# Optimization experiments

Hardware: AMD Instinct MI355X
Metric: run time of the kernel (lower is better)

The kernel has to match this reference:

```python
import jax, jax.numpy as jnp
import numpy as np
import math

B, H, W, DM = 4, 64, 64, 96
DS, DCONV, EXPAND = 16, 3, 2
DI = EXPAND * DM
DTR = math.ceil(DM / 16)
K = 4
HID = 4 * DI


def layernorm(x, g, b, eps=1e-5):
    m = x.mean(-1, keepdims=True)
    v = ((x - m) ** 2).mean(-1, keepdims=True)
    return (x - m) / jnp.sqrt(v + eps) * g + b


def dwconv(x, w, b=None):
    # x: (B,C,H,W), w: (C,1,kh,kw) depthwise, odd kernel => SAME padding == k//2
    out = jax.lax.conv_general_dilated(x, w, (1, 1), 'SAME',
                                       feature_group_count=x.shape[1],
                                       dimension_numbers=('NCHW', 'OIHW', 'NCHW'))
    if b is not None:
        out = out + b[None, :, None, None]
    return out


def ss2d_core(xc, x_proj_w, dt_projs_w, dt_projs_b, A_logs, Ds):
    # xc: (b, d_inner, h, w) -> (b, d_inner, L) summed over 4 scan directions
    b, c, h, w = xc.shape
    L = h * w
    x_hw = xc.reshape(b, c, L)
    x_wh = xc.transpose(0, 1, 3, 2).reshape(b, c, L)
    xs = jnp.stack([x_hw, x_wh], axis=1)                 # (b,2,c,L)
    xs = jnp.concatenate([xs, jnp.flip(xs, -1)], axis=1)  # (b,4,c,L)
    x_dbl = jnp.einsum('bkdl,kcd->bkcl', xs, x_proj_w)
    dts, Bs, Cs = jnp.split(x_dbl, [DTR, DTR + DS], axis=2)
    dts = jnp.einsum('bkrl,kdr->bkdl', dts, dt_projs_w)
    delta = jax.nn.softplus(dts + dt_projs_b[None, :, :, None])  # (b,K,c,L)
    A = -jnp.exp(A_logs).reshape(K, c, DS)                       # (K,c,n)

    def step(hst, inp):
        x_t, d_t, B_t, C_t = inp  # (b,K,c),(b,K,c),(b,K,n),(b,K,n)
        dA = jnp.exp(d_t[..., None] * A)                       # (b,K,c,n)
        hst = hst * dA + (d_t * x_t)[..., None] * B_t[:, :, None, :]
        y = jnp.einsum('bkdn,bkn->bkd', hst, C_t)
        return hst, y

    seq = (jnp.moveaxis(xs, -1, 0), jnp.moveaxis(delta, -1, 0),
           jnp.moveaxis(Bs, -1, 0), jnp.moveaxis(Cs, -1, 0))
    h0 = jnp.zeros((b, K, c, DS), xc.dtype)
    _, ys = jax.lax.scan(step, h0, seq)          # (L,b,K,c)
    ys = jnp.moveaxis(ys, 0, -1)                 # (b,K,c,L)
    ys = ys + Ds.reshape(K, c)[None, :, :, None] * xs
    y1 = ys[:, 0]
    inv = jnp.flip(ys[:, 2:4], -1)
    y2 = inv[:, 0]
    wh = ys[:, 1].reshape(b, c, w, h).swapaxes(2, 3).reshape(b, c, L)
    invwh = inv[:, 1].reshape(b, c, w, h).swapaxes(2, 3).reshape(b, c, L)
    return y1 + y2 + wh + invwh


def msffn(y, in_w, in_b, dw1, dw3, dw5, ln_g, ln_b, out_w, out_b):
    hcl = jax.nn.silu(y @ in_w.T + in_b)          # (b,h,w,HID)
    hc = hcl.transpose(0, 3, 1, 2)
    hc = hc + dwconv(hc, dw1) + dwconv(hc, dw3) + dwconv(hc, dw5)
    hn = layernorm(hc.transpose(0, 2, 3, 1), ln_g, ln_b)
    return hn @ out_w.T + out_b


def setup_inputs() -> dict:
    key = jax.random.key(0)
    ks = jax.random.split(key, 16)
    dt_init_std = DTR ** -0.5
    dt = jnp.exp(jax.random.uniform(ks[0], (K, DI)) * (math.log(0.1) - math.log(0.001)) + math.log(0.001))
    dt = jnp.clip(dt, 1e-4, None)
    inv_dt = dt + jnp.log(-jnp.expm1(-dt))          # softplus-inverse init for dt bias
    A_logs = jnp.tile(jnp.log(jnp.arange(1, DS + 1, dtype=jnp.float32))[None, :], (K * DI, 1))
    r = lambda i, sh, s: jax.random.normal(ks[i], sh, jnp.float32) * s
    return {
        'x': r(1, (B, H, W, DM), 1.0),
        'in_proj_w': r(2, (2 * DI, DM), DM ** -0.5),
        'conv_w': r(3, (DI, 1, DCONV, DCONV), 0.2),
        'conv_b': jnp.zeros((DI,), jnp.float32),
        'x_proj_w': r(4, (K, DTR + 2 * DS, DI), DI ** -0.5),
        'dt_projs_w': jax.random.uniform(ks[5], (K, DI, DTR), minval=-dt_init_std, maxval=dt_init_std),
        'dt_projs_b': inv_dt,
        'A_logs': A_logs,
        'Ds': jnp.ones((K * DI,), jnp.float32),
        'out_norm_g': jnp.ones((DI,), jnp.float32),
        'out_norm_b': jnp.zeros((DI,), jnp.float32),
        'out_proj_w': r(6, (DM, DI), DI ** -0.5),
        'ffn_in_w': r(7, (HID, DI), DI ** -0.5),
        'ffn_in_b': jnp.zeros((HID,), jnp.float32),
        'ffn_dw1': r(8, (HID, 1, 1, 1), 0.3),
        'ffn_dw3': r(9, (HID, 1, 3, 3), 0.2),
        'ffn_dw5': r(10, (HID, 1, 5, 5), 0.1),
        'ffn_ln_g': jnp.ones((HID,), jnp.float32),
        'ffn_ln_b': jnp.zeros((HID,), jnp.float32),
        'ffn_out_w': r(11, (DM, HID), HID ** -0.5),
        'ffn_out_b': jnp.zeros((DM,), jnp.float32),
        'skip_scale': jnp.ones((1,), jnp.float32),
    }


def reference(x, in_proj_w, conv_w, conv_b, x_proj_w, dt_projs_w, dt_projs_b, A_logs, Ds,
              out_norm_g, out_norm_b, out_proj_w, ffn_in_w, ffn_in_b, ffn_dw1, ffn_dw3,
              ffn_dw5, ffn_ln_g, ffn_ln_b, ffn_out_w, ffn_out_b, skip_scale):
    b, h, w, _ = x.shape
    xz = x @ in_proj_w.T                          # (b,h,w,2*DI)
    xi, z = jnp.split(xz, 2, axis=-1)
    xc = jax.nn.silu(dwconv(xi.transpose(0, 3, 1, 2), conv_w, conv_b))  # (b,DI,h,w)
    y = ss2d_core(xc, x_proj_w, dt_projs_w, dt_projs_b, A_logs, Ds)     # (b,DI,L)
    y = y.swapaxes(1, 2).reshape(b, h, w, DI)
    y = layernorm(y, out_norm_g, out_norm_b)
    y = y * jax.nn.silu(z)
    out = y @ out_proj_w.T
    ffn = msffn(y, ffn_in_w, ffn_in_b, ffn_dw1, ffn_dw3, ffn_dw5,
                ffn_ln_g, ffn_ln_b, ffn_out_w, ffn_out_b)
    return out + skip_scale * ffn
```

## Files before the change

### kernel.cpp

```cpp
#include <hip/hip_runtime.h>
#include <hip/hip_bf16.h>

constexpr int BB = 4, HH = 64, WW = 64, DMv = 96;
constexpr int DSn = 16, DIv = 192, DTRv = 6, KKv = 4, HIDv = 768;
constexpr int LL = 4096;
constexpr int NC = 64, CHK = LL / NC;
constexpr int NR = BB * LL;
constexpr int XDS = 40;

constexpr size_t S_xi   = (size_t)BB * LL * DIv;
constexpr size_t S_xdbl = (size_t)BB * KKv * LL * XDS;
constexpr size_t S_big  = (size_t)BB * KKv * LL * DIv;
constexpr size_t S_sp   = (size_t)BB * KKv * NC * DIv * DSn;

typedef __attribute__((ext_vector_type(8))) short short8;
typedef __attribute__((ext_vector_type(4))) short short4v;
typedef __attribute__((ext_vector_type(4))) float floatx4;

__device__ __forceinline__ float sigf(float x) { return 1.f / (1.f + __expf(-x)); }
__device__ __forceinline__ float softp(float x) {
  return (x > 20.f) ? x : __logf(1.f + __expf(x));
}
__device__ __forceinline__ short bfbits(float v) {
  __hip_bfloat16 h = __float2bfloat16(v);
  return *(short*)&h;
}

__device__ __forceinline__ int lmap(int k, int l) {
  int lr = (k & 2) ? (LL - 1 - l) : l;
  return (k & 1) ? (((lr & 63) << 6) | (lr >> 6)) : lr;
}

__global__ void k_wprep(const float* __restrict__ fiw, const float* __restrict__ opw,
                        const float* __restrict__ fow, const float* __restrict__ in_w,
                        const float* __restrict__ xpw, const float* __restrict__ x,
                        float* __restrict__ wt, float* __restrict__ xt,
                        short* __restrict__ fiwP, short* __restrict__ opwP,
                        short* __restrict__ fowP, short* __restrict__ wcatP) {
  int bx = blockIdx.x, t = threadIdx.x;
  __shared__ float smbuf[32 * 65];
  if (bx < 36) {
    int r0 = (bx / 3) * 32, c0 = (bx % 3) * 32;
    float (*tile)[33] = (float(*)[33])smbuf;
    int tc = t & 31, tr = t >> 5;
#pragma unroll
    for (int i = 0; i < 4; ++i)
      tile[tr + i * 8][tc] = in_w[(size_t)(r0 + tr + i * 8) * 96 + c0 + tc];
    __syncthreads();
#pragma unroll
    for (int i = 0; i < 4; ++i)
      wt[(size_t)(c0 + tr + i * 8) * 384 + r0 + tc] = tile[tc][tr + i * 8];
    return;
  }
  if (bx < 804) {
    int i4 = bx - 36;
    int r0 = (i4 / 3) * 64, k0 = (i4 % 3) * 32;
    float (*tile)[65] = (float(*)[65])smbuf;
#pragma unroll
    for (int ii = 0; ii < 8; ++ii) {
      int i = (t >> 5) + ii * 8, j = t & 31;
      tile[j][i] = x[(size_t)(r0 + i) * 96 + k0 + j];
    }
    __syncthreads();
#pragma unroll
    for (int jj = 0; jj < 8; ++jj) {
      int j = (t >> 6) + jj * 4, i = t & 63;
      xt[(size_t)(k0 + j) * NR + r0 + i] = tile[j][i];
    }
    return;
  }
  int lane = t & 63, ln16 = lane & 15, qd = lane >> 4;
  if (bx < 876) {
    int f = (bx - 804) * 4 + (t >> 6);
    int kt = f / 48, ntg = f % 48;
    int n = ntg * 16 + ln16;
#pragma unroll
    for (int j = 0; j < 8; ++j) {
      int k = kt * 32 + qd * 8 + j;
      fiwP[(size_t)f * 512 + lane * 8 + j] = bfbits(fiw[(size_t)n * DIv + k]);
    }
    return;
  }
  if (bx < 894) {
    int u = (bx - 876) * 4 + (t >> 6);
    int f = u >> 1, part = u & 1;
    int kt = f / 6, ntg = f % 6;
    int n = ntg * 16 + ln16;
#pragma unroll
    for (int j = 0; j < 8; ++j) {
      int k = kt * 32 + qd * 8 + j;
      float w = opw[(size_t)n * DIv + k];
      __hip_bfloat16 h = __float2bfloat16(w);
      float v = part ? (w - (float)h) : w;
      opwP[((size_t)(part * 36 + f)) * 512 + lane * 8 + j] = bfbits(v);
    }
    return;
  }
  if (bx < 966) {
    int u = (bx - 894) * 4 + (t >> 6);
    int f = u >> 1, part = u & 1;
    int kt = f / 6, ntg = f % 6;
    int n = ntg * 16 + ln16;
#pragma unroll
    for (int j = 0; j < 8; ++j) {
      int k = kt * 32 + qd * 8 + j;
      float w = fow[(size_t)n * HIDv + k];
      __hip_bfloat16 h = __float2bfloat16(w);
      float v = part ? (w - (float)h) : w;
      fowP[((size_t)(part * 144 + f)) * 512 + lane * 8 + j] = bfbits(v);
    }
    return;
  }
  {
    int u = (bx - 966) * 4 + (t >> 6);
    int p = u / 60, r = u % 60;
    int part = r / 30, r2 = r % 30;
    int kt = r2 / 5, g = r2 % 5;
    int n = g * 16 + ln16;
#pragma unroll
    for (int j = 0; j < 8; ++j) {
      int kd = kt * 32 + qd * 8 + j;
      float w = 0.f;
      if (n < 76) {
        int ksel = ((n >= 38) ? 2 : 0) + p;
        int cc = (n >= 38) ? n - 38 : n;
        w = xpw[(size_t)(ksel * 38 + cc) * DIv + kd];
      }
      __hip_bfloat16 h = __float2bfloat16(w);
      float v = part ? (w - (float)h) : w;
      wcatP[((size_t)(((p * 2 + part) * 6 + kt) * 5 + g)) * 512 + lane * 8 + j] = bfbits(v);
    }
  }
}

__global__ void k_inproj(const float* __restrict__ xt, const float* __restrict__ wt,
                         float* __restrict__ xi, float* __restrict__ z) {
  int t = threadIdx.x;
  int wv = t >> 6, lane = t & 63;
  int rq = blockIdx.x * 256 + wv * 64 + lane;
  int c0 = blockIdx.y * 8;
  const float4* xt4 = (const float4*)xt;
  float4 acc[8];
#pragma unroll
  for (int c = 0; c < 8; ++c) acc[c] = make_float4(0.f, 0.f, 0.f, 0.f);
  for (int k = 0; k < 96; ++k) {
    float4 xv = xt4[(size_t)k * (NR / 4) + rq];
    const float* wr = wt + k * 384 + c0;
#pragma unroll
    for (int c = 0; c < 8; ++c) {
      float w = wr[c];
      acc[c].x += w * xv.x; acc[c].y += w * xv.y;
      acc[c].z += w * xv.z; acc[c].w += w * xv.w;
    }
  }
  float* dst; int cc;
  if (c0 < DIv) { dst = xi; cc = c0; } else { dst = z; cc = c0 - DIv; }
#pragma unroll
  for (int li = 0; li < 4; ++li) {
    size_t row = (size_t)rq * 4 + li;
    float4 v0, v1;
    v0.x = (&acc[0].x)[li]; v0.y = (&acc[1].x)[li];
    v0.z = (&acc[2].x)[li]; v0.w = (&acc[3].x)[li];
    v1.x = (&acc[4].x)[li]; v1.y = (&acc[5].x)[li];
    v1.z = (&acc[6].x)[li]; v1.w = (&acc[7].x)[li];
    float4* o4 = (float4*)(dst + row * DIv + cc);
    o4[0] = v0; o4[1] = v1;
  }
}

constexpr int TW2 = 18;
__global__ void k_dwconv3(const float* __restrict__ xi, const float* __restrict__ cw,
                          const float* __restrict__ cb, float* __restrict__ xc,
                          short* __restrict__ xcBh, short* __restrict__ xcBl) {
  int tile = blockIdx.x;
  int cg = blockIdx.y, b = blockIdx.z;
  int t = threadIdx.x;
  int ti0 = (tile >> 2) * 16, tj0 = (tile & 3) * 16;
  __shared__ float sm[TW2 * TW2 * 32];

  for (int e = t; e < TW2 * TW2 * 32; e += 256) {
    int ec = e & 31;
    int sp = e >> 5;
    int hi = sp / TW2, hj = sp % TW2;
    int gi = ti0 + hi - 1, gj = tj0 + hj - 1;
    float v = 0.f;
    if ((unsigned)gi < (unsigned)HH && (unsigned)gj < (unsigned)WW)
      v = xi[((size_t)b * LL + gi * WW + gj) * DIv + cg * 32 + ec];
    sm[e] = v;
  }

  int c = t & 31, s0 = t >> 5;
  int cglob = cg * 32 + c;
  float wc[9];
#pragma unroll
  for (int j = 0; j < 9; ++j) wc[j] = cw[cglob * 9 + j];
  float bv = cb[cglob];
  __syncthreads();

  float res[32];
  for (int i = 0; i < 32; ++i) {
    int p = s0 + (i << 3);
    int r = p >> 4, q = p & 15;
    float s = bv;
#pragma unroll
    for (int di = 0; di < 3; ++di)
#pragma unroll
      for (int dj = 0; dj < 3; ++dj)
        s += sm[((r + di) * TW2 + (q + dj)) * 32 + c] * wc[di * 3 + dj];
    res[i] = s * sigf(s);
  }
  __syncthreads();
  for (int i = 0; i < 32; ++i) {
    int p = s0 + (i << 3);
    sm[p * 35 + c] = res[i];
  }
  __syncthreads();
  for (int it = 0; it < 32; ++it) {
    int e = it * 256 + t;
    int p = e >> 5, ec = e & 31;
    int l = (ti0 + (p >> 4)) * WW + tj0 + (p & 15);
    float v = sm[p * 35 + ec];
    size_t idx = ((size_t)b * LL + l) * DIv + cg * 32 + ec;
    xc[idx] = v;
    __hip_bfloat16 hh = __float2bfloat16(v);
    xcBh[idx] = *(short*)&hh;
    xcBl[idx] = bfbits(v - (float)hh);
  }
}

__global__ void k_xdblmf(const short* __restrict__ xcBh, const short* __restrict__ xcBl,
                         const short* __restrict__ wcatP, float* __restrict__ xdbl) {
  int t = threadIdx.x;
  int wv = t >> 6, lane = t & 63;
  int ln16 = lane & 15, qd = lane >> 4;
  int pb = blockIdx.y;
  int p = pb >> 2, b = pb & 3;
  int m0 = blockIdx.x * 64 + wv * 16;
  int r = m0 + ln16;
  int l = p ? (((r & 63) << 6) | (r >> 6)) : r;
  const short* ah = xcBh + ((size_t)(b * LL + l)) * DIv + qd * 8;
  const short* al = xcBl + ((size_t)(b * LL + l)) * DIv + qd * 8;
  floatx4 acc[5];
  floatx4 zero4 = {0.f, 0.f, 0.f, 0.f};
#pragma unroll
  for (int g = 0; g < 5; ++g) acc[g] = zero4;
#pragma unroll
  for (int kt = 0; kt < 6; ++kt) {
    short8 Ah = *(const short8*)(ah + kt * 32);
    short8 Al = *(const short8*)(al + kt * 32);
    const short* bh = wcatP + ((size_t)(((p * 2 + 0) * 6 + kt) * 5)) * 512 + lane * 8;
    const short* bl = wcatP + ((size_t)(((p * 2 + 1) * 6 + kt) * 5)) * 512 + lane * 8;
#pragma unroll
    for (int g = 0; g < 5; ++g) {
      short8 Bh = *(const short8*)(bh + (size_t)g * 512);
      short8 Bl = *(const short8*)(bl + (size_t)g * 512);
      acc[g] = __builtin_amdgcn_mfma_f32_16x16x32_bf16(Ah, Bh, acc[g], 0, 0, 0);
      acc[g] = __builtin_amdgcn_mfma_f32_16x16x32_bf16(Al, Bh, acc[g], 0, 0, 0);
      acc[g] = __builtin_amdgcn_mfma_f32_16x16x32_bf16(Ah, Bl, acc[g], 0, 0, 0);
    }
  }
#pragma unroll
  for (int g = 0; g < 5; ++g) {
    int col = g * 16 + ln16;
    if (col < 76) {
#pragma unroll
      for (int rr = 0; rr < 4; ++rr) {
        int rowr = m0 + qd * 4 + rr;
        int kk = (col >= 38) ? (2 + p) : p;
        int cc = (col >= 38) ? col - 38 : col;
        int lpos = (col >= 38) ? (LL - 1 - rowr) : rowr;
        int phys = cc + (cc >= 6 ? 2 : 0);
        size_t ro = (((size_t)(b * KKv + kk)) * LL + lpos) * XDS;
        xdbl[ro + phys] = acc[g][rr];
        if (col == 5) { xdbl[ro + 6] = 0.f; xdbl[ro + 7] = 0.f; }
      }
    }
  }
}

__global__ void k_scan1(const float* __restrict__ xdbl, const float* __restrict__ xc,
                        const float* __restrict__ alogs, const float* __restrict__ dtw,
                        const float* __restrict__ dtb,
                        float* __restrict__ S, float* __restrict__ P) {
  int bx = blockIdx.x;
  int c = bx / 3, dblk = bx % 3;
  int k = blockIdx.y, b = blockIdx.z;
  int t = threadIdx.x, dl = t >> 2, nq = t & 3;
  int d = dblk * 64 + dl;
  __shared__ float de_s[16][64], xv_s[16][64], bc_s[16][16];
  float A[4];
#pragma unroll
  for (int j = 0; j < 4; ++j)
    A[j] = -__expf(alogs[(size_t)(k * DIv + d) * DSn + nq * 4 + j]);
  int derow = t >> 4, dec0 = (t & 15) * 4;
  float DTW[4][6], DTB[4];
#pragma unroll
  for (int jj = 0; jj < 4; ++jj) {
    int dd = k * DIv + dblk * 64 + dec0 + jj;
    DTB[jj] = dtb[dd];
#pragma unroll
    for (int r2 = 0; r2 < 6; ++r2) DTW[jj][r2] = dtw[(size_t)dd * 6 + r2];
  }
  size_t bkL = (size_t)(b * KKv + k) * LL;
  const float* xq = xdbl + bkL * XDS;
  const float* xcb = xc + (size_t)b * LL * DIv;
  float h[4] = {0.f, 0.f, 0.f, 0.f}, sA[4] = {0.f, 0.f, 0.f, 0.f};
  int l0 = c * CHK;
  for (int tile = 0; tile < CHK / 16; ++tile) {
    int lt = l0 + tile * 16;
    __syncthreads();
    {
      int r = t >> 4, q = t & 15;
      int lc = lmap(k, lt + r);
      *(float4*)&xv_s[r][q * 4] = *(const float4*)(xcb + (size_t)lc * DIv + dblk * 64 + q * 4);
      if (t < 64) {
        int r2 = t >> 2, q2 = t & 3;
        *(float4*)&bc_s[r2][q2 * 4] = *(const float4*)(xq + (size_t)(lt + r2) * XDS + 8 + q2 * 4);
      }
      const float* dtp = xq + (size_t)(lt + derow) * XDS;
      float d0 = dtp[0], d1 = dtp[1], d2 = dtp[2], d3 = dtp[3], d4 = dtp[4], d5 = dtp[5];
#pragma unroll
      for (int jj = 0; jj < 4; ++jj) {
        float s = DTB[jj] + d0 * DTW[jj][0] + d1 * DTW[jj][1] + d2 * DTW[jj][2]
                          + d3 * DTW[jj][3] + d4 * DTW[jj][4] + d5 * DTW[jj][5];
        de_s[derow][dec0 + jj] = softp(s);
      }
    }
    __syncthreads();
#pragma unroll
    for (int i2 = 0; i2 < 16; ++i2) {
      float de = de_s[i2][dl];
      float xv = xv_s[i2][dl];
      float4 Bv = *(float4*)&bc_s[i2][nq * 4];
      float db = de * xv;
#pragma unroll
      for (int j = 0; j < 4; ++j) {
        float u = de * A[j];
        sA[j] += u;
        h[j] = h[j] * __expf(u) + db * (&Bv.x)[j];
      }
    }
  }
  size_t o = ((((size_t)(b * KKv + k) * NC + c) * 3 + dblk) * 1024) + (size_t)t * 4;
  float4 hs, ps;
#pragma unroll
  for (int j = 0; j < 4; ++j) { (&hs.x)[j] = h[j]; (&ps.x)[j] = __expf(sA[j]); }
  *(float4*)(S + o) = hs;
  *(float4*)(P + o) = ps;
}

__global__ void k_scan2(float* __restrict__ S, const float* __restrict__ P) {
  int dblk = blockIdx.x, k = blockIdx.y, b = blockIdx.z;
  int t = threadIdx.x;
  size_t base = (((size_t)(b * KKv + k) * NC) * 3 + dblk) * 1024 + (size_t)t * 4;
  float4 h = make_float4(0.f, 0.f, 0.f, 0.f);
  for (int c = 0; c < NC; ++c) {
    size_t o = base + (size_t)c * 3 * 1024;
    float4 s = *(float4*)(S + o), p = *(float4*)(P + o);
    *(float4*)(S + o) = h;
    h.x = s.x + p.x * h.x; h.y = s.y + p.y * h.y;
    h.z = s.z + p.z * h.z; h.w = s.w + p.w * h.w;
  }
}

__global__ void k_scan3(const float* __restrict__ xdbl, const float* __restrict__ xc,
                        const float* __restrict__ alogs, const float* __restrict__ dtw,
                        const float* __restrict__ dtb,
                        const float* __restrict__ Hin, float* __restrict__ ys) {
  int bx = blockIdx.x;
  int c = bx / 3, dblk = bx % 3;
  int k = blockIdx.y, b = blockIdx.z;
  int t = threadIdx.x, dl = t >> 2, nq = t & 3;
  int d = dblk * 64 + dl;
  __shared__ float de_s[16][64], xv_s[16][64], bc_s[16][32];
  float A[4];
#pragma unroll
  for (int j = 0; j < 4; ++j)
    A[j] = -__expf(alogs[(size_t)(k * DIv + d) * DSn + nq * 4 + j]);
  int derow = t >> 4, dec0 = (t & 15) * 4;
  float DTW[4][6], DTB[4];
#pragma unroll
  for (int jj = 0; jj < 4; ++jj) {
    int dd = k * DIv + dblk * 64 + dec0 + jj;
    DTB[jj] = dtb[dd];
#pragma unroll
    for (int r2 = 0; r2 < 6; ++r2) DTW[jj][r2] = dtw[(size_t)dd * 6 + r2];
  }
  size_t bkL = (size_t)(b * KKv + k) * LL;
  const float* xq = xdbl + bkL * XDS;
  const float* xcb = xc + (size_t)b * LL * DIv;
  float* yp = ys + bkL * DIv + d;
  size_t o = ((((size_t)(b * KKv + k) * NC + c) * 3 + dblk) * 1024) + (size_t)t * 4;
  float4 h4 = *(const float4*)(Hin + o);
  float h[4] = {h4.x, h4.y, h4.z, h4.w};
  int l0 = c * CHK;
  for (int tile = 0; tile < CHK / 16; ++tile) {
    int lt = l0 + tile * 16;
    __syncthreads();
    {
      int r = t >> 4, q = t & 15;
      int lc = lmap(k, lt + r);
      *(float4*)&xv_s[r][q * 4] = *(const float4*)(xcb + (size_t)lc * DIv + dblk * 64 + q * 4);
      if (t < 128) {
        int r2 = t >> 3, q2 = t & 7;
        *(float4*)&bc_s[r2][q2 * 4] = *(const float4*)(xq + (size_t)(lt + r2) * XDS + 8 + q2 * 4);
      }
      const float* dtp = xq + (size_t)(lt + derow) * XDS;
      float d0 = dtp[0], d1 = dtp[1], d2 = dtp[2], d3 = dtp[3], d4 = dtp[4], d5 = dtp[5];
#pragma unroll
      for (int jj = 0; jj < 4; ++jj) {
        float s = DTB[jj] + d0 * DTW[jj][0] + d1 * DTW[jj][1] + d2 * DTW[jj][2]
                          + d3 * DTW[jj][3] + d4 * DTW[jj][4] + d5 * DTW[jj][5];
        de_s[derow][dec0 + jj] = softp(s);
      }
    }
    __syncthreads();
#pragma unroll
    for (int i2 = 0; i2 < 16; ++i2) {
      float de = de_s[i2][dl];
      float xv = xv_s[i2][dl];
      float4 Bv = *(float4*)&bc_s[i2][nq * 4];
      float4 Cv = *(float4*)&bc_s[i2][16 + nq * 4];
      float db = de * xv;
      float p = 0.f;
#pragma unroll
      for (int j = 0; j < 4; ++j) {
        h[j] = h[j] * __expf(de * A[j]) + db * (&Bv.x)[j];
        p += h[j] * (&Cv.x)[j];
      }
      p += __shfl_down(p, 2, 4);
      p += __shfl_down(p, 1, 4);
      if (nq == 0) yp[(size_t)(lt + i2) * DIv] = p;
    }
  }
}

__global__ void k_comlnt(const float* __restrict__ ys, const float* __restrict__ xc,
                         const float* __restrict__ Ds, const float* __restrict__ z,
                         const float* __restrict__ g, const float* __restrict__ be,
                         __hip_bfloat16* __restrict__ ygtB,
                         __hip_bfloat16* __restrict__ ygtBl) {
  int bl0 = blockIdx.x * 32;
  int b = bl0 >> 12, l0 = bl0 & 4095;
  int t = threadIdx.x;
  __shared__ float vbuf[32 * 193];
  __shared__ float m_[32], rs_[32];
  {
    int grp = t >> 6, lane6 = t & 63;
    size_t base = (size_t)b * KKv * LL * DIv;
#pragma unroll
    for (int i8 = 0; i8 < 8; ++i8) {
      int li = grp + i8 * 4;
      int l = l0 + li;
      int lT = ((l & 63) << 6) | (l >> 6);
      const float* r0 = ys + base + (size_t)l * DIv;
      const float* r2 = ys + base + ((size_t)2 * LL + (LL - 1 - l)) * DIv;
      const float* r1 = ys + base + ((size_t)1 * LL + lT) * DIv;
      const float* r3 = ys + base + ((size_t)3 * LL + (LL - 1 - lT)) * DIv;
      const float* xr = xc + ((size_t)b * LL + l) * DIv;
#pragma unroll
      for (int cc = 0; cc < 3; ++cc) {
        int d = lane6 + cc * 64;
        float sd = Ds[d] + Ds[DIv + d] + Ds[2 * DIv + d] + Ds[3 * DIv + d];
        vbuf[li * 193 + d] = r0[d] + r2[d] + r1[d] + r3[d] + sd * xr[d];
      }
    }
  }
  __syncthreads();
  {
    int r = t >> 3, q = t & 7;
    float s = 0.f, qq = 0.f;
#pragma unroll
    for (int j = 0; j < 24; ++j) {
      float v = vbuf[r * 193 + q + j * 8];
      s += v; qq += v * v;
    }
    s += __shfl_down(s, 4, 8); qq += __shfl_down(qq, 4, 8);
    s += __shfl_down(s, 2, 8); qq += __shfl_down(qq, 2, 8);
    s += __shfl_down(s, 1, 8); qq += __shfl_down(qq, 1, 8);
    if (q == 0) {
      float m = s / DIv;
      m_[r] = m;
      rs_[r] = rsqrtf(qq / DIv - m * m + 1e-5f);
    }
  }
  __syncthreads();
  int tc = t & 31, tr = t >> 5;
#pragma unroll
  for (int ch = 0; ch < 6; ++ch) {
    int c0 = ch * 32;
    float gg = g[c0 + tc], bb = be[c0 + tc];
#pragma unroll
    for (int i = 0; i < 4; ++i) {
      int r = tr + i * 8;
      float v = vbuf[r * 193 + c0 + tc];
      float zz = z[(size_t)(bl0 + r) * DIv + c0 + tc];
      float val = (v - m_[r]) * rs_[r] * gg + bb;
      float gated = val * zz * sigf(zz);
      __hip_bfloat16 h = __float2bfloat16(gated);
      ygtB[(size_t)(bl0 + r) * DIv + c0 + tc] = h;
      ygtBl[(size_t)(bl0 + r) * DIv + c0 + tc] = __float2bfloat16(gated - (float)h);
    }
  }
}

__global__ void k_ffnmf(const __hip_bfloat16* __restrict__ ygtB,
                        const short* __restrict__ fiwP,
                        const float* __restrict__ bias, float* __restrict__ hcl) {
  int t = threadIdx.x;
  int wv = t >> 6, lane = t & 63;
  int ln16 = lane & 15, qd = lane >> 4;
  int m0 = blockIdx.x * 64 + wv * 16;
  int n0 = blockIdx.y * 64;
  int ntg0 = n0 >> 4;
  floatx4 acc[4];
  floatx4 zero4 = {0.f, 0.f, 0.f, 0.f};
#pragma unroll
  for (int nt = 0; nt < 4; ++nt) acc[nt] = zero4;
  const short* arow = (const short*)ygtB + (size_t)(m0 + ln16) * DIv + qd * 8;
#pragma unroll
  for (int kt = 0; kt < 6; ++kt) {
    short8 a = *(const short8*)(arow + kt * 32);
    const short* bb = fiwP + ((size_t)(kt * 48 + ntg0) * 64 + lane) * 8;
#pragma unroll
    for (int nt = 0; nt < 4; ++nt) {
      short8 bfr = *(const short8*)(bb + (size_t)nt * 512);
      acc[nt] = __builtin_amdgcn_mfma_f32_16x16x32_bf16(a, bfr, acc[nt], 0, 0, 0);
    }
  }
#pragma unroll
  for (int nt = 0; nt < 4; ++nt) {
    int col = n0 + nt * 16 + ln16;
    float bv = bias[col];
#pragma unroll
    for (int r = 0; r < 4; ++r) {
      int row = m0 + qd * 4 + r;
      float s = acc[nt][r] + bv;
      hcl[(size_t)row * HIDv + col] = s * sigf(s);
    }
  }
}

constexpr int TS = 16, CG = 32, TW = TS + 4;
__global__ void k_ffnconv2(const float* __restrict__ hcl, const float* __restrict__ w1,
                           const float* __restrict__ w3, const float* __restrict__ w5,
                           float* __restrict__ hc2) {
  int tile = blockIdx.x;
  int cg = blockIdx.y, b = blockIdx.z;
  int t = threadIdx.x;
  int ti0 = (tile >> 2) * TS, tj0 = (tile & 3) * TS;
  __shared__ float sm[TW * TW * CG];

  for (int e = t; e < TW * TW * CG; e += 256) {
    int ec = e & 31;
    int sp = e >> 5;
    int hi = sp / TW, hj = sp % TW;
    int gi = ti0 + hi - 2, gj = tj0 + hj - 2;
    float v = 0.f;
    if ((unsigned)gi < (unsigned)HH && (unsigned)gj < (unsigned)WW)
      v = hcl[((size_t)b * LL + gi * WW + gj) * HIDv + cg * CG + ec];
    sm[e] = v;
  }

  int c = t & 31;
  int cglob = cg * CG + c;
  float wc[25];
#pragma unroll
  for (int di = 0; di < 5; ++di)
#pragma unroll
    for (int dj = 0; dj < 5; ++dj) {
      float w = w5[cglob * 25 + di * 5 + dj];
      if (di >= 1 && di <= 3 && dj >= 1 && dj <= 3)
        w += w3[cglob * 9 + (di - 1) * 3 + (dj - 1)];
      if (di == 2 && dj == 2) w += 1.f + w1[cglob];
      wc[di * 5 + dj] = w;
    }
  __syncthreads();

  int q2 = t >> 5;
#pragma unroll
  for (int half = 0; half < 2; ++half) {
    int q = q2 + half * 8;
    float win[5][5];
#pragma unroll
    for (int di = 0; di < 4; ++di)
#pragma unroll
      for (int dj = 0; dj < 5; ++dj)
        win[di][dj] = sm[(di * TW + (q + dj)) * CG + c];
#pragma unroll
    for (int r = 0; r < 16; ++r) {
      int slot = (r + 4) % 5;
#pragma unroll
      for (int dj = 0; dj < 5; ++dj)
        win[slot][dj] = sm[(((r + 4) * TW) + (q + dj)) * CG + c];
      float s = 0.f;
#pragma unroll
      for (int di = 0; di < 5; ++di) {
        int wsl = (r + di) % 5;
#pragma unroll
        for (int dj = 0; dj < 5; ++dj)
          s += win[wsl][dj] * wc[di * 5 + dj];
      }
      hc2[((size_t)b * LL + (ti0 + r) * WW + (tj0 + q)) * HIDv + cglob] = s;
    }
  }
}

constexpr int LNROWS = 16, LNPAD = 776;
__global__ void k_ln2b(const float* __restrict__ hc2, const float* __restrict__ g,
                       const float* __restrict__ be,
                       short* __restrict__ hnBh, short* __restrict__ hnBl) {
  int r0 = blockIdx.x * LNROWS;
  int t = threadIdx.x;
  __shared__ float rows[LNROWS * LNPAD];
  __shared__ float m_[LNROWS], rs_[LNROWS];
#pragma unroll
  for (int i = 0; i < 12; ++i) {
    int idx4 = t + i * 256;
    int row = idx4 / 192, c4 = idx4 % 192;
    float4 v = *(const float4*)(hc2 + (size_t)(r0 + row) * HIDv + c4 * 4);
    *(float4*)&rows[row * LNPAD + c4 * 4] = v;
  }
  __syncthreads();
  {
    int r = t >> 4, q = t & 15;
    float s = 0.f, qq = 0.f;
#pragma unroll
    for (int j = 0; j < 48; ++j) {
      float v = rows[r * LNPAD + q + j * 16];
      s += v; qq += v * v;
    }
    s += __shfl_down(s, 8, 16); qq += __shfl_down(qq, 8, 16);
    s += __shfl_down(s, 4, 16); qq += __shfl_down(qq, 4, 16);
    s += __shfl_down(s, 2, 16); qq += __shfl_down(qq, 2, 16);
    s += __shfl_down(s, 1, 16); qq += __shfl_down(qq, 1, 16);
    if (q == 0) {
      float m = s / HIDv;
      m_[r] = m;
      rs_[r] = rsqrtf(qq / HIDv - m * m + 1e-5f);
    }
  }
  __syncthreads();
#pragma unroll
  for (int i = 0; i < 12; ++i) {
    int idx4 = t + i * 256;
    int row = idx4 / 192, c4 = idx4 % 192;
    float4 v = *(const float4*)&rows[row * LNPAD + c4 * 4];
    float4 gv = *(const float4*)(g + c4 * 4);
    float4 bv = *(const float4*)(be + c4 * 4);
    float m = m_[row], rs = rs_[row];
    short4v hh, ll;
#pragma unroll
    for (int j = 0; j < 4; ++j) {
      float val = ((&v.x)[j] - m) * rs * (&gv.x)[j] + (&bv.x)[j];
      __hip_bfloat16 h = __float2bfloat16(val);
      hh[j] = *(short*)&h;
      ll[j] = bfbits(val - (float)h);
    }
    size_t o = (size_t)(r0 + row) * HIDv + c4 * 4;
    *(short4v*)(hnBh + o) = hh;
    *(short4v*)(hnBl + o) = ll;
  }
}

__global__ void k_finalmf(const short* __restrict__ hnBh, const short* __restrict__ hnBl,
                          const short* __restrict__ fowP,
                          const short* __restrict__ ygtBh, const short* __restrict__ ygtBl,
                          const short* __restrict__ opwP,
                          const float* __restrict__ fob, const float* __restrict__ skip,
                          float* __restrict__ dout) {
  int t = threadIdx.x;
  int wv = t >> 6, lane = t & 63;
  int ln16 = lane & 15, qd = lane >> 4;
  int m0 = blockIdx.x * 64 + wv * 16;
  floatx4 accF[6], accO[6];
  floatx4 zero4 = {0.f, 0.f, 0.f, 0.f};
#pragma unroll
  for (int nt = 0; nt < 6; ++nt) { accF[nt] = zero4; accO[nt] = zero4; }
  const short* arh = hnBh + (size_t)(m0 + ln16) * HIDv + qd * 8;
  const short* arl = hnBl + (size_t)(m0 + ln16) * HIDv + qd * 8;
#pragma unroll 2
  for (int kt = 0; kt < 24; ++kt) {
    short8 ah = *(const short8*)(arh + kt * 32);
    short8 al = *(const short8*)(arl + kt * 32);
    const short* bh = fowP + ((size_t)(kt * 6) * 64 + lane) * 8;
    const short* bl = fowP + ((size_t)(144 + kt * 6) * 64 + lane) * 8;
#pragma unroll
    for (int nt = 0; nt < 6; ++nt) {
      short8 bhv = *(const short8*)(bh + (size_t)nt * 512);
      short8 blv = *(const short8*)(bl + (size_t)nt * 512);
      accF[nt] = __builtin_amdgcn_mfma_f32_16x16x32_bf16(ah, bhv, accF[nt], 0, 0, 0);
      accF[nt] = __builtin_amdgcn_mfma_f32_16x16x32_bf16(al, bhv, accF[nt], 0, 0, 0);
      accF[nt] = __builtin_amdgcn_mfma_f32_16x16x32_bf16(ah, blv, accF[nt], 0, 0, 0);
    }
  }
  const short* orh = ygtBh + (size_t)(m0 + ln16) * DIv + qd * 8;
  const short* orl = ygtBl + (size_t)(m0 + ln16) * DIv + qd * 8;
#pragma unroll 2
  for (int kt = 0; kt < 6; ++kt) {
    short8 ah = *(const short8*)(orh + kt * 32);
    short8 al = *(const short8*)(orl + kt * 32);
    const short* bh = opwP + ((size_t)(kt * 6) * 64 + lane) * 8;
    const short* bl = opwP + ((size_t)(36 + kt * 6) * 64 + lane) * 8;
#pragma unroll
    for (int nt = 0; nt < 6; ++nt) {
      short8 bhv = *(const short8*)(bh + (size_t)nt * 512);
      short8 blv = *(const short8*)(bl + (size_t)nt * 512);
      accO[nt] = __builtin_amdgcn_mfma_f32_16x16x32_bf16(ah, bhv, accO[nt], 0, 0, 0);
      accO[nt] = __builtin_amdgcn_mfma_f32_16x16x32_bf16(al, bhv, accO[nt], 0, 0, 0);
      accO[nt] = __builtin_amdgcn_mfma_f32_16x16x32_bf16(ah, blv, accO[nt], 0, 0, 0);
    }
  }
  float sk = skip[0];
#pragma unroll
  for (int nt = 0; nt < 6; ++nt) {
    int col = nt * 16 + ln16;
    float bv = fob[col];
#pragma unroll
    for (int r = 0; r < 4; ++r) {
      int row = m0 + qd * 4 + r;
      dout[(size_t)row * DMv + col] = accO[nt][r] + sk * (accF[nt][r] + bv);
    }
  }
}

extern "C" void kernel_launch(void* const* d_in, const int* in_sizes, int n_in,
                              void* d_out, int out_size, void* d_ws, size_t ws_size,
                              hipStream_t stream) {
  const float* x        = (const float*)d_in[0];
  const float* in_w     = (const float*)d_in[1];
  const float* conv_w   = (const float*)d_in[2];
  const float* conv_b   = (const float*)d_in[3];
  const float* xpw      = (const float*)d_in[4];
  const float* dtw      = (const float*)d_in[5];
  const float* dtb      = (const float*)d_in[6];
  const float* alogs    = (const float*)d_in[7];
  const float* Ds       = (const float*)d_in[8];
  const float* ong      = (const float*)d_in[9];
  const float* onb      = (const float*)d_in[10];
  const float* opw      = (const float*)d_in[11];
  const float* fiw      = (const float*)d_in[12];
  const float* fib      = (const float*)d_in[13];
  const float* dw1      = (const float*)d_in[14];
  const float* dw3      = (const float*)d_in[15];
  const float* dw5      = (const float*)d_in[16];
  const float* flg      = (const float*)d_in[17];
  const float* flb      = (const float*)d_in[18];
  const float* fow      = (const float*)d_in[19];
  const float* fob      = (const float*)d_in[20];
  const float* skip     = (const float*)d_in[21];

  float* ws    = (float*)d_ws;
  float* xi    = ws;
  float* z     = xi + S_xi;
  float* xc    = z + S_xi;
  float* xdbl  = xc + S_xi;
  float* scr   = xdbl + S_xdbl;
  float* ys    = scr + S_big;
  float* wtiny = ys + S_big;
  float* wt    = wtiny;
  __hip_bfloat16* ygtB = (__hip_bfloat16*)(wt + 36864);
  short* fiwP  = (short*)(wt + 36864) + (size_t)NR * DIv;
  short* opwP  = fiwP + 288 * 512;
  short* fowP  = opwP + 2 * 36 * 512;
  short* wcatP = fowP + 2 * 144 * 512;

  float* xt = scr;
  k_wprep<<<996, 256, 0, stream>>>(fiw, opw, fow, in_w, xpw, x,
                                   wt, xt, fiwP, opwP, fowP, wcatP);

  dim3 gip(NR / 1024, 48);
  k_inproj<<<gip, 256, 0, stream>>>(xt, wt, xi, z);

  short* xcBh = (short*)ys;
  short* xcBl = xcBh + (size_t)NR * DIv;
  dim3 gdw(16, DIv / 32, BB);
  k_dwconv3<<<gdw, 256, 0, stream>>>(xi, conv_w, conv_b, xc, xcBh, xcBl);

  dim3 gxd(LL / 64, 8);
  k_xdblmf<<<gxd, 256, 0, stream>>>(xcBh, xcBl, wcatP, xdbl);

  float* Sbuf = scr;
  float* Pbuf = scr + S_sp;
  dim3 gs13(NC * 3, KKv, BB);
  dim3 gs2(3, KKv, BB);
  k_scan1<<<gs13, 256, 0, stream>>>(xdbl, xc, alogs, dtw, dtb, Sbuf, Pbuf);
  k_scan2<<<gs2, 256, 0, stream>>>(Sbuf, Pbuf);
  k_scan3<<<gs13, 256, 0, stream>>>(xdbl, xc, alogs, dtw, dtb, Sbuf, ys);

  __hip_bfloat16* ygtBl = (__hip_bfloat16*)xi;
  k_comlnt<<<NR / 32, 256, 0, stream>>>(ys, xc, Ds, z, ong, onb, ygtB, ygtBl);

  float* hcl = scr;
  dim3 gmf(NR / 64, HIDv / 64);
  k_ffnmf<<<gmf, 256, 0, stream>>>(ygtB, fiwP, fib, hcl);

  float* hc2 = ys;
  dim3 gc(16, HIDv / CG, BB);
  k_ffnconv2<<<gc, 256, 0, stream>>>(hcl, dw1, dw3, dw5, hc2);

  short* hnBh = (short*)scr;
  short* hnBl = hnBh + (size_t)NR * HIDv;
  k_ln2b<<<NR / LNROWS, 256, 0, stream>>>(hc2, flg, flb, hnBh, hnBl);

  k_finalmf<<<NR / 64, 256, 0, stream>>>(hnBh, hnBl, fowP,
                                         (const short*)ygtB, (const short*)ygtBl, opwP,
                                         fob, skip, (float*)d_out);
}
```

Baseline: 419.7 us.

## Shrink per-block work in LN, conv kernels and split-K the final GEMM

Several kernels get smaller per-block tiles so more blocks launch: the combine+layernorm kernel drops from 32 to 8 rows per block, the FFN depthwise conv handles 16 channels per block with one column per thread, and the second layernorm handles 8 rows per block. The final fused GEMM is split along K into two blocks per row tile. Each half writes partials into the freed z buffer, and a new merge kernel adds them. The aim is better occupancy and load balance, at the cost of an extra launch plus extra partial-result traffic and more redundant halo/weight loads.

```diff
diff --git a/kernel.cpp b/kernel.cpp
--- a/kernel.cpp
+++ b/kernel.cpp
@@ -440,44 +440,42 @@
                          const float* __restrict__ g, const float* __restrict__ be,
                          __hip_bfloat16* __restrict__ ygtB,
                          __hip_bfloat16* __restrict__ ygtBl) {
-  int bl0 = blockIdx.x * 32;
+  int bl0 = blockIdx.x * 8;
   int b = bl0 >> 12, l0 = bl0 & 4095;
   int t = threadIdx.x;
-  __shared__ float vbuf[32 * 193];
-  __shared__ float m_[32], rs_[32];
+  __shared__ float vbuf[8 * 193];
+  __shared__ float m_[8], rs_[8];
   {
-    int grp = t >> 6, lane6 = t & 63;
+    int li = t >> 5, lane32 = t & 31;
     size_t base = (size_t)b * KKv * LL * DIv;
-#pragma unroll
-    for (int i8 = 0; i8 < 8; ++i8) {
-      int li = grp + i8 * 4;
-      int l = l0 + li;
-      int lT = ((l & 63) << 6) | (l >> 6);
-      const float* r0 = ys + base + (size_t)l * DIv;
-      const float* r2 = ys + base + ((size_t)2 * LL + (LL - 1 - l)) * DIv;
-      const float* r1 = ys + base + ((size_t)1 * LL + lT) * DIv;
-      const float* r3 = ys + base + ((size_t)3 * LL + (LL - 1 - lT)) * DIv;
-      const float* xr = xc + ((size_t)b * LL + l) * DIv;
-#pragma unroll
-      for (int cc = 0; cc < 3; ++cc) {
-        int d = lane6 + cc * 64;
-        float sd = Ds[d] + Ds[DIv + d] + Ds[2 * DIv + d] + Ds[3 * DIv + d];
-        vbuf[li * 193 + d] = r0[d] + r2[d] + r1[d] + r3[d] + sd * xr[d];
-      }
+    int l = l0 + li;
+    int lT = ((l & 63) << 6) | (l >> 6);
+    const float* r0 = ys + base + (size_t)l * DIv;
+    const float* r2 = ys + base + ((size_t)2 * LL + (LL - 1 - l)) * DIv;
+    const float* r1 = ys + base + ((size_t)1 * LL + lT) * DIv;
+    const float* r3 = ys + base + ((size_t)3 * LL + (LL - 1 - lT)) * DIv;
+    const float* xr = xc + ((size_t)b * LL + l) * DIv;
+#pragma unroll
+    for (int cc = 0; cc < 6; ++cc) {
+      int d = lane32 + cc * 32;
+      float sd = Ds[d] + Ds[DIv + d] + Ds[2 * DIv + d] + Ds[3 * DIv + d];
+      vbuf[li * 193 + d] = r0[d] + r2[d] + r1[d] + r3[d] + sd * xr[d];
     }
   }
   __syncthreads();
   {
-    int r = t >> 3, q = t & 7;
+    int r = t >> 5, q = t & 31;
     float s = 0.f, qq = 0.f;
 #pragma unroll
-    for (int j = 0; j < 24; ++j) {
-      float v = vbuf[r * 193 + q + j * 8];
+    for (int j = 0; j < 6; ++j) {
+      float v = vbuf[r * 193 + q + j * 32];
       s += v; qq += v * v;
     }
-    s += __shfl_down(s, 4, 8); qq += __shfl_down(qq, 4, 8);
-    s += __shfl_down(s, 2, 8); qq += __shfl_down(qq, 2, 8);
-    s += __shfl_down(s, 1, 8); qq += __shfl_down(qq, 1, 8);
+    s += __shfl_down(s, 16, 32); qq += __shfl_down(qq, 16, 32);
+    s += __shfl_down(s, 8, 32);  qq += __shfl_down(qq, 8, 32);
+    s += __shfl_down(s, 4, 32);  qq += __shfl_down(qq, 4, 32);
+    s += __shfl_down(s, 2, 32);  qq += __shfl_down(qq, 2, 32);
+    s += __shfl_down(s, 1, 32);  qq += __shfl_down(qq, 1, 32);
     if (q == 0) {
       float m = s / DIv;
       m_[r] = m;
@@ -490,17 +488,13 @@
   for (int ch = 0; ch < 6; ++ch) {
     int c0 = ch * 32;
     float gg = g[c0 + tc], bb = be[c0 + tc];
-#pragma unroll
-    for (int i = 0; i < 4; ++i) {
-      int r = tr + i * 8;
-      float v = vbuf[r * 193 + c0 + tc];
-      float zz = z[(size_t)(bl0 + r) * DIv + c0 + tc];
-      float val = (v - m_[r]) * rs_[r] * gg + bb;
-      float gated = val * zz * sigf(zz);
-      __hip_bfloat16 h = __float2bfloat16(gated);
-      ygtB[(size_t)(bl0 + r) * DIv + c0 + tc] = h;
-      ygtBl[(size_t)(bl0 + r) * DIv + c0 + tc] = __float2bfloat16(gated - (float)h);
-    }
+    float v = vbuf[tr * 193 + c0 + tc];
+    float zz = z[(size_t)(bl0 + tr) * DIv + c0 + tc];
+    float val = (v - m_[tr]) * rs_[tr] * gg + bb;
+    float gated = val * zz * sigf(zz);
+    __hip_bfloat16 h = __float2bfloat16(gated);
+    ygtB[(size_t)(bl0 + tr) * DIv + c0 + tc] = h;
+    ygtBl[(size_t)(bl0 + tr) * DIv + c0 + tc] = __float2bfloat16(gated - (float)h);
   }
 }
 
@@ -541,7 +535,7 @@
   }
 }
 
-constexpr int TS = 16, CG = 32, TW = TS + 4;
+constexpr int TS = 16, CG = 16, TW = TS + 4;
 __global__ void k_ffnconv2(const float* __restrict__ hcl, const float* __restrict__ w1,
                            const float* __restrict__ w3, const float* __restrict__ w5,
                            float* __restrict__ hc2) {
@@ -552,8 +546,8 @@
   __shared__ float sm[TW * TW * CG];
 
   for (int e = t; e < TW * TW * CG; e += 256) {
-    int ec = e & 31;
-    int sp = e >> 5;
+    int ec = e & 15;
+    int sp = e >> 4;
     int hi = sp / TW, hj = sp % TW;
     int gi = ti0 + hi - 2, gj = tj0 + hj - 2;
     float v = 0.f;
@@ -562,7 +556,8 @@
     sm[e] = v;
   }
 
-  int c = t & 31;
+  int c = t & 15;
+  int q = t >> 4;
   int cglob = cg * CG + c;
   float wc[25];
 #pragma unroll
@@ -577,36 +572,31 @@
     }
   __syncthreads();
 
-  int q2 = t >> 5;
-#pragma unroll
-  for (int half = 0; half < 2; ++half) {
-    int q = q2 + half * 8;
-    float win[5][5];
-#pragma unroll
-    for (int di = 0; di < 4; ++di)
+  float win[5][5];
+#pragma unroll
+  for (int di = 0; di < 4; ++di)
+#pragma unroll
+    for (int dj = 0; dj < 5; ++dj)
+      win[di][dj] = sm[(di * TW + (q + dj)) * CG + c];
+#pragma unroll
+  for (int r = 0; r < 16; ++r) {
+    int slot = (r + 4) % 5;
+#pragma unroll
+    for (int dj = 0; dj < 5; ++dj)
+      win[slot][dj] = sm[(((r + 4) * TW) + (q + dj)) * CG + c];
+    float s = 0.f;
+#pragma unroll
+    for (int di = 0; di < 5; ++di) {
+      int wsl = (r + di) % 5;
 #pragma unroll
       for (int dj = 0; dj < 5; ++dj)
-        win[di][dj] = sm[(di * TW + (q + dj)) * CG + c];
-#pragma unroll
-    for (int r = 0; r < 16; ++r) {
-      int slot = (r + 4) % 5;
-#pragma unroll
-      for (int dj = 0; dj < 5; ++dj)
-        win[slot][dj] = sm[(((r + 4) * TW) + (q + dj)) * CG + c];
-      float s = 0.f;
-#pragma unroll
-      for (int di = 0; di < 5; ++di) {
-        int wsl = (r + di) % 5;
-#pragma unroll
-        for (int dj = 0; dj < 5; ++dj)
-          s += win[wsl][dj] * wc[di * 5 + dj];
-      }
-      hc2[((size_t)b * LL + (ti0 + r) * WW + (tj0 + q)) * HIDv + cglob] = s;
-    }
-  }
-}
-
-constexpr int LNROWS = 16, LNPAD = 776;
+        s += win[wsl][dj] * wc[di * 5 + dj];
+    }
+    hc2[((size_t)b * LL + (ti0 + r) * WW + (tj0 + q)) * HIDv + cglob] = s;
+  }
+}
+
+constexpr int LNROWS = 8, LNPAD = 776;
 __global__ void k_ln2b(const float* __restrict__ hc2, const float* __restrict__ g,
                        const float* __restrict__ be,
                        short* __restrict__ hnBh, short* __restrict__ hnBl) {
@@ -615,7 +605,7 @@
   __shared__ float rows[LNROWS * LNPAD];
   __shared__ float m_[LNROWS], rs_[LNROWS];
 #pragma unroll
-  for (int i = 0; i < 12; ++i) {
+  for (int i = 0; i < 6; ++i) {
     int idx4 = t + i * 256;
     int row = idx4 / 192, c4 = idx4 % 192;
     float4 v = *(const float4*)(hc2 + (size_t)(r0 + row) * HIDv + c4 * 4);
@@ -623,17 +613,18 @@
   }
   __syncthreads();
   {
-    int r = t >> 4, q = t & 15;
+    int r = t >> 5, q = t & 31;
     float s = 0.f, qq = 0.f;
 #pragma unroll
-    for (int j = 0; j < 48; ++j) {
-      float v = rows[r * LNPAD + q + j * 16];
+    for (int j = 0; j < 24; ++j) {
+      float v = rows[r * LNPAD + q + j * 32];
       s += v; qq += v * v;
     }
-    s += __shfl_down(s, 8, 16); qq += __shfl_down(qq, 8, 16);
-    s += __shfl_down(s, 4, 16); qq += __shfl_down(qq, 4, 16);
-    s += __shfl_down(s, 2, 16); qq += __shfl_down(qq, 2, 16);
-    s += __shfl_down(s, 1, 16); qq += __shfl_down(qq, 1, 16);
+    s += __shfl_down(s, 16, 32); qq += __shfl_down(qq, 16, 32);
+    s += __shfl_down(s, 8, 32);  qq += __shfl_down(qq, 8, 32);
+    s += __shfl_down(s, 4, 32);  qq += __shfl_down(qq, 4, 32);
+    s += __shfl_down(s, 2, 32);  qq += __shfl_down(qq, 2, 32);
+    s += __shfl_down(s, 1, 32);  qq += __shfl_down(qq, 1, 32);
     if (q == 0) {
       float m = s / HIDv;
       m_[r] = m;
@@ -642,7 +633,7 @@
   }
   __syncthreads();
 #pragma unroll
-  for (int i = 0; i < 12; ++i) {
+  for (int i = 0; i < 6; ++i) {
     int idx4 = t + i * 256;
     int row = idx4 / 192, c4 = idx4 % 192;
     float4 v = *(const float4*)&rows[row * LNPAD + c4 * 4];
@@ -668,19 +659,21 @@
                           const short* __restrict__ ygtBh, const short* __restrict__ ygtBl,
                           const short* __restrict__ opwP,
                           const float* __restrict__ fob, const float* __restrict__ skip,
-                          float* __restrict__ dout) {
+                          float* __restrict__ part) {
   int t = threadIdx.x;
   int wv = t >> 6, lane = t & 63;
   int ln16 = lane & 15, qd = lane >> 4;
   int m0 = blockIdx.x * 64 + wv * 16;
-  floatx4 accF[6], accO[6];
+  int ks = blockIdx.y;
+  floatx4 accF[6];
   floatx4 zero4 = {0.f, 0.f, 0.f, 0.f};
 #pragma unroll
-  for (int nt = 0; nt < 6; ++nt) { accF[nt] = zero4; accO[nt] = zero4; }
+  for (int nt = 0; nt < 6; ++nt) accF[nt] = zero4;
   const short* arh = hnBh + (size_t)(m0 + ln16) * HIDv + qd * 8;
   const short* arl = hnBl + (size_t)(m0 + ln16) * HIDv + qd * 8;
+  int kt0 = ks * 12;
 #pragma unroll 2
-  for (int kt = 0; kt < 24; ++kt) {
+  for (int kt = kt0; kt < kt0 + 12; ++kt) {
     short8 ah = *(const short8*)(arh + kt * 32);
     short8 al = *(const short8*)(arl + kt * 32);
     const short* bh = fowP + ((size_t)(kt * 6) * 64 + lane) * 8;
@@ -694,34 +687,59 @@
       accF[nt] = __builtin_amdgcn_mfma_f32_16x16x32_bf16(ah, blv, accF[nt], 0, 0, 0);
     }
   }
-  const short* orh = ygtBh + (size_t)(m0 + ln16) * DIv + qd * 8;
-  const short* orl = ygtBl + (size_t)(m0 + ln16) * DIv + qd * 8;
+  float sk = skip[0];
+  if (ks == 0) {
+    floatx4 accO[6];
+#pragma unroll
+    for (int nt = 0; nt < 6; ++nt) accO[nt] = zero4;
+    const short* orh = ygtBh + (size_t)(m0 + ln16) * DIv + qd * 8;
+    const short* orl = ygtBl + (size_t)(m0 + ln16) * DIv + qd * 8;
 #pragma unroll 2
-  for (int kt = 0; kt < 6; ++kt) {
-    short8 ah = *(const short8*)(orh + kt * 32);
-    short8 al = *(const short8*)(orl + kt * 32);
-    const short* bh = opwP + ((size_t)(kt * 6) * 64 + lane) * 8;
-    const short* bl = opwP + ((size_t)(36 + kt * 6) * 64 + lane) * 8;
+    for (int kt = 0; kt < 6; ++kt) {
+      short8 ah = *(const short8*)(orh + kt * 32);
+      short8 al = *(const short8*)(orl + kt * 32);
+      const short* bh = opwP + ((size_t)(kt * 6) * 64 + lane) * 8;
+      const short* bl = opwP + ((size_t)(36 + kt * 6) * 64 + lane) * 8;
+#pragma unroll
+      for (int nt = 0; nt < 6; ++nt) {
+        short8 bhv = *(const short8*)(bh + (size_t)nt * 512);
+        short8 blv = *(const short8*)(bl + (size_t)nt * 512);
+        accO[nt] = __builtin_amdgcn_mfma_f32_16x16x32_bf16(ah, bhv, accO[nt], 0, 0, 0);
+        accO[nt] = __builtin_amdgcn_mfma_f32_16x16x32_bf16(al, bhv, accO[nt], 0, 0, 0);
+        accO[nt] = __builtin_amdgcn_mfma_f32_16x16x32_bf16(ah, blv, accO[nt], 0, 0, 0);
+      }
+    }
 #pragma unroll
     for (int nt = 0; nt < 6; ++nt) {
-      short8 bhv = *(const short8*)(bh + (size_t)nt * 512);
-      short8 blv = *(const short8*)(bl + (size_t)nt * 512);
-      accO[nt] = __builtin_amdgcn_mfma_f32_16x16x32_bf16(ah, bhv, accO[nt], 0, 0, 0);
-      accO[nt] = __builtin_amdgcn_mfma_f32_16x16x32_bf16(al, bhv, accO[nt], 0, 0, 0);
-      accO[nt] = __builtin_amdgcn_mfma_f32_16x16x32_bf16(ah, blv, accO[nt], 0, 0, 0);
-    }
-  }
-  float sk = skip[0];
-#pragma unroll
-  for (int nt = 0; nt < 6; ++nt) {
-    int col = nt * 16 + ln16;
-    float bv = fob[col];
-#pragma unroll
-    for (int r = 0; r < 4; ++r) {
-      int row = m0 + qd * 4 + r;
-      dout[(size_t)row * DMv + col] = accO[nt][r] + sk * (accF[nt][r] + bv);
-    }
-  }
+      int col = nt * 16 + ln16;
+#pragma unroll
+      for (int r = 0; r < 4; ++r) {
+        int row = m0 + qd * 4 + r;
+        part[(size_t)row * DMv + col] = accO[nt][r] + sk * accF[nt][r];
+      }
+    }
+  } else {
+#pragma unroll
+    for (int nt = 0; nt < 6; ++nt) {
+      int col = nt * 16 + ln16;
+      float bv = fob[col];
+#pragma unroll
+      for (int r = 0; r < 4; ++r) {
+        int row = m0 + qd * 4 + r;
+        part[(size_t)NR * DMv + (size_t)row * DMv + col] = sk * (accF[nt][r] + bv);
+      }
+    }
+  }
+}
+
+__global__ void k_finmerge(const float* __restrict__ part, float* __restrict__ dout) {
+  size_t i = (size_t)blockIdx.x * 256 + threadIdx.x;
+  const float4* p4 = (const float4*)part;
+  size_t npart = (size_t)NR * DMv / 4;
+  float4 a = p4[i], b = p4[i + npart];
+  float4 r;
+  r.x = a.x + b.x; r.y = a.y + b.y; r.z = a.z + b.z; r.w = a.w + b.w;
+  ((float4*)dout)[i] = r;
 }
 
 extern "C" void kernel_launch(void* const* d_in, const int* in_sizes, int n_in,
@@ -789,7 +807,7 @@
   k_scan3<<<gs13, 256, 0, stream>>>(xdbl, xc, alogs, dtw, dtb, Sbuf, ys);
 
   __hip_bfloat16* ygtBl = (__hip_bfloat16*)xi;
-  k_comlnt<<<NR / 32, 256, 0, stream>>>(ys, xc, Ds, z, ong, onb, ygtB, ygtBl);
+  k_comlnt<<<NR / 8, 256, 0, stream>>>(ys, xc, Ds, z, ong, onb, ygtB, ygtBl);
 
   float* hcl = scr;
   dim3 gmf(NR / 64, HIDv / 64);
@@ -803,7 +821,10 @@
   short* hnBl = hnBh + (size_t)NR * HIDv;
   k_ln2b<<<NR / LNROWS, 256, 0, stream>>>(hc2, flg, flb, hnBh, hnBl);
 
-  k_finalmf<<<NR / 64, 256, 0, stream>>>(hnBh, hnBl, fowP,
-                                         (const short*)ygtB, (const short*)ygtBl, opwP,
-                                         fob, skip, (float*)d_out);
-}
+  float* partbuf = z;
+  dim3 gfm(NR / 64, 2);
+  k_finalmf<<<gfm, 256, 0, stream>>>(hnBh, hnBl, fowP,
+                                     (const short*)ygtB, (const short*)ygtBl, opwP,
+                                     fob, skip, partbuf);
+  k_finmerge<<<(NR * DMv / 4) / 256, 256, 0, stream>>>(partbuf, (float*)d_out);
+}
```

New measurement: 393.6 us. 6.2% less time.
